# Optimization experiments

Measured on AMD Instinct MI355X. Metric: run time of the kernel, lower is better.

## Reference

```python
import jax, jax.numpy as jnp
import numpy as np

B, S0, S1 = 4, 768, 256
T = S0 + S1
D0, D1 = 2048, 1024
N, K, H = 8, 1, 256  # num_heads, num_kv_heads, head_dim
G = N // K
BIG_NEG = -2.3819763e38


def _apply_rope(x, positions, max_wavelength=10000):
    # x: [B, L, Hn, Hd]; positions: [B, L] float32
    half = x.shape[-1] // 2
    freq_exponents = (2.0 / x.shape[-1]) * jnp.arange(half, dtype=jnp.float32)
    timescale = max_wavelength ** freq_exponents
    radians = positions[..., None] / timescale[None, None, :]   # [B, L, half]
    radians = radians[..., None, :]                             # [B, L, 1, half]
    sin, cos = jnp.sin(radians), jnp.cos(radians)
    x1, x2 = jnp.split(x, 2, axis=-1)
    res = jnp.concatenate([x1 * cos - x2 * sin, x2 * cos + x1 * sin], axis=-1)
    return res.astype(x.dtype)


def setup_inputs() -> dict:
    key = jax.random.key(0)
    ks = jax.random.split(key, 8)
    x0 = jax.random.normal(ks[0], (B, S0, D0), dtype=jnp.float32)
    x1 = jax.random.normal(ks[1], (B, S1, D1), dtype=jnp.float32)
    positions = jnp.broadcast_to(jnp.arange(T, dtype=jnp.float32), (B, T))
    # causal mask [B, 1, T, T]
    attn_mask = jnp.broadcast_to(jnp.tril(jnp.ones((T, T), dtype=bool)), (B, 1, T, T))
    # lecun_normal-style init: std = 1/sqrt(fan_in=width)
    q0_w = jax.random.normal(ks[2], (N, D0, H), dtype=jnp.float32) * (D0 ** -0.5)
    kv0_w = jax.random.normal(ks[3], (2, K, D0, H), dtype=jnp.float32) * (D0 ** -0.5)
    q1_w = jax.random.normal(ks[4], (N, D1, H), dtype=jnp.float32) * (D1 ** -0.5)
    kv1_w = jax.random.normal(ks[5], (2, K, D1, H), dtype=jnp.float32) * (D1 ** -0.5)
    o0_w = jax.random.normal(ks[6], (N, H, D0), dtype=jnp.float32) * ((N * H) ** -0.5)
    o1_w = jax.random.normal(ks[7], (N, H, D1), dtype=jnp.float32) * ((N * H) ** -0.5)
    return {"x0": x0, "x1": x1, "positions": positions, "attn_mask": attn_mask,
            "q0_w": q0_w, "kv0_w": kv0_w, "q1_w": q1_w, "kv1_w": kv1_w,
            "o0_w": o0_w, "o1_w": o1_w}


def reference(x0, x1, positions, attn_mask, q0_w, kv0_w, q1_w, kv1_w, o0_w, o1_w):
    dtype = x0.dtype
    # per-stream GQA projections (num_kv_heads != num_heads path)
    q_a = jnp.einsum('BTD,NDH->BTNH', x0, q0_w)
    kv_a = jnp.einsum('BSD,CKDH->CBSKH', x0, kv0_w)
    q_b = jnp.einsum('BTD,NDH->BTNH', x1, q1_w)
    kv_b = jnp.einsum('BSD,CKDH->CBSKH', x1, kv1_w)
    # concat streams along sequence
    q = jnp.concatenate([q_a, q_b], axis=1)                 # [B, T, N, H]
    k = jnp.concatenate([kv_a[0], kv_b[0]], axis=1)         # [B, T, K, H]
    v = jnp.concatenate([kv_a[1], kv_b[1]], axis=1)         # [B, T, K, H]
    # inline RoPE + query scaling
    q = _apply_rope(q, positions) * (H ** -0.5)
    k = _apply_rope(k, positions)
    # GQA grouping: N = K * G
    qg = q.reshape(q.shape[0], q.shape[1], K, G, H)          # [B, T, K, G, H]
    logits = jnp.einsum('BTKGH,BSKH->BKGTS', qg, k,
                        preferred_element_type=jnp.float32)  # fp32 scores
    masked = jnp.where(attn_mask[:, :, None, :, :], logits, BIG_NEG)
    probs = jax.nn.softmax(masked, axis=-1).astype(dtype)
    encoded = jnp.einsum('BKGTS,BSKH->BTKGH', probs, v)
    encoded = encoded.reshape(encoded.shape[0], encoded.shape[1], N, H)  # [B, T, N, H]
    out0 = jnp.einsum('BTNH,NHD->BTD', encoded[:, :S0], o0_w)
    out1 = jnp.einsum('BTNH,NHD->BTD', encoded[:, S0:], o1_w)
    return (out0, out1)
```

## Files before the change

### kernel.cpp

```cpp
#include <hip/hip_runtime.h>

typedef unsigned short u16;
typedef __attribute__((ext_vector_type(8))) short bf16x8;
typedef __attribute__((ext_vector_type(4))) float f32x4;

#define CB   4
#define CS0  768
#define CS1  256
#define CT   1024
#define CD0  2048
#define CD1  1024
#define CN   8
#define CH   256
#define IDENT (1 << 30)
#define BIGBASE 0x7fffffff

__device__ __forceinline__ float bf2f(u16 u) {
    union { unsigned int i; float f; } v;
    v.i = ((unsigned int)u) << 16;
    return v.f;
}
__device__ __forceinline__ u16 f2bf(float f) {
    union { float f; unsigned int i; } v;
    v.f = f;
    unsigned int r = 0x7fffu + ((v.i >> 16) & 1u);
    return (u16)((v.i + r) >> 16);
}

__device__ __forceinline__ void gl_lds16(const u16* g, u16* lds_base) {
    __builtin_amdgcn_global_load_lds(
        (const __attribute__((address_space(1))) void*)g,
        (__attribute__((address_space(3))) void*)lds_base,
        16, 0, 0);
}

struct PSeg { const float* in; u16* out; int R, C, base, lgx, lgy, mode; };
struct PSeg8 { PSeg t[8]; };

__global__ __launch_bounds__(256) void prep_multi(PSeg8 segs)
{
    __shared__ float tl[2][32][33];
    int bid = blockIdx.x;
    PSeg g = segs.t[0];
    #pragma unroll
    for (int i = 1; i < 8; i++)
        if (bid >= segs.t[i].base) g = segs.t[i];
    int r = bid - g.base;
    int tid = threadIdx.x;
    if (g.mode == 0) {
        int i = r * 512 + tid;
        float4 v0 = ((const float4*)g.in)[i];
        float4 v1 = ((const float4*)g.in)[i + 256];
        ushort4 o0, o1;
        o0.x = f2bf(v0.x); o0.y = f2bf(v0.y); o0.z = f2bf(v0.z); o0.w = f2bf(v0.w);
        o1.x = f2bf(v1.x); o1.y = f2bf(v1.y); o1.z = f2bf(v1.z); o1.w = f2bf(v1.w);
        ((ushort4*)g.out)[i] = o0;
        ((ushort4*)g.out)[i + 256] = o1;
    } else {
        int bx  = r & ((1 << g.lgx) - 1);
        int byh = (r >> g.lgx) & ((1 << (g.lgy - 1)) - 1);
        int bz  = r >> (g.lgx + g.lgy - 1);
        const float* in = g.in + (size_t)bz * g.R * g.C;
        u16* out = g.out + (size_t)bz * g.R * g.C;
        int c0 = bx * 32, r0 = byh * 64;
        int lty = tid >> 3, ltx = tid & 7;
        #pragma unroll
        for (int tt = 0; tt < 2; tt++) {
            float4 v = *(const float4*)&in[(size_t)(r0 + tt * 32 + lty) * g.C + c0 + ltx * 4];
            tl[tt][lty][ltx * 4 + 0] = v.x;
            tl[tt][lty][ltx * 4 + 1] = v.y;
            tl[tt][lty][ltx * 4 + 2] = v.z;
            tl[tt][lty][ltx * 4 + 3] = v.w;
        }
        __syncthreads();
        int uy = tid >> 3, ux = tid & 7;
        int tt2 = ux >> 2, a0 = (ux & 3) * 8;
        bf16x8 ov;
        #pragma unroll
        for (int k = 0; k < 8; k++)
            ((u16*)&ov)[k] = f2bf(tl[tt2][a0 + k][uy]);
        *(bf16x8*)&out[(size_t)(c0 + uy) * g.R + r0 + ux * 8] = ov;
    }
}

struct GSeg {
    const u16* A; const u16* BT; void* C;
    int K, Cstride, base, lgnx;
    int Sa, Ta, ta, Sc, Tc, tc, obf, pad;
};
struct GSeg4 { GSeg s[4]; };

__global__ __launch_bounds__(256, 3) void gemm128_multi(GSeg4 segs)
{
    __shared__ __align__(16) u16 lds[3 * 8192];

    int bid = blockIdx.x;
    GSeg g = segs.s[0];
    if (bid >= segs.s[1].base) g = segs.s[1];
    if (bid >= segs.s[2].base) g = segs.s[2];
    if (bid >= segs.s[3].base) g = segs.s[3];

    int tid  = threadIdx.x;
    int r    = bid - g.base;
    int n0   = (r & ((1 << g.lgnx) - 1)) * 128;
    int m0   = (r >> g.lgnx) * 128;
    int wave = tid >> 6, lane = tid & 63;

    int srow  = tid >> 2;
    int skoff = ((tid & 3) ^ ((srow >> 1) & 3)) * 8;
    int am1 = m0 + srow, am2 = m0 + 64 + srow;
    const u16* aptr1 = g.A + (size_t)((am1 / g.Sa) * g.Ta + g.ta + am1 % g.Sa) * g.K + skoff;
    const u16* aptr2 = g.A + (size_t)((am2 / g.Sa) * g.Ta + g.ta + am2 % g.Sa) * g.K + skoff;
    const u16* bptr1 = g.BT + (size_t)(n0 + srow) * g.K + skoff;
    const u16* bptr2 = g.BT + (size_t)(n0 + 64 + srow) * g.K + skoff;

    int mw = (wave >> 1) * 64, nw = (wave & 1) * 64;
    int l15 = lane & 15;
    int q4  = lane >> 4;
    int sw  = (q4 ^ ((l15 >> 1) & 3)) * 8;

#define STAGE(bufi, tt) do { int kk = (tt) * 32; \
        u16* base = lds + (bufi) * 8192 + wave * 512; \
        gl_lds16(aptr1 + kk, base); \
        gl_lds16(aptr2 + kk, base + 2048); \
        gl_lds16(bptr1 + kk, base + 4096); \
        gl_lds16(bptr2 + kk, base + 6144); } while (0)

    f32x4 acc[4][4] = {};
    int nkt = g.K >> 5;

    STAGE(0, 0);
    STAGE(1, 1);

    int cur = 0, nxt = 2;
    for (int t = 0; t < nkt; ++t) {
        if (t + 1 < nkt) asm volatile("s_waitcnt vmcnt(4)" ::: "memory");
        else             asm volatile("s_waitcnt vmcnt(0)" ::: "memory");
        __builtin_amdgcn_sched_barrier(0);
        __builtin_amdgcn_s_barrier();
        asm volatile("" ::: "memory");
        if (t + 2 < nkt) STAGE(nxt, t + 2);

        const u16* At = lds + cur * 8192;
        const u16* Bt = At + 4096;
        bf16x8 af[4], bfr[4];
        #pragma unroll
        for (int i = 0; i < 4; i++)
            af[i] = *(const bf16x8*)&At[(mw + i * 16 + l15) * 32 + sw];
        #pragma unroll
        for (int i = 0; i < 4; i++)
            bfr[i] = *(const bf16x8*)&Bt[(nw + i * 16 + l15) * 32 + sw];
        asm volatile("s_waitcnt lgkmcnt(0)" ::: "memory");
        __builtin_amdgcn_sched_barrier(0);
        __builtin_amdgcn_s_setprio(1);
        #pragma unroll
        for (int mi = 0; mi < 4; mi++)
            #pragma unroll
            for (int ni = 0; ni < 4; ni++)
                acc[mi][ni] = __builtin_amdgcn_mfma_f32_16x16x32_bf16(
                    af[mi], bfr[ni], acc[mi][ni], 0, 0, 0);
        __builtin_amdgcn_s_setprio(0);
        cur = (cur == 2) ? 0 : cur + 1;
        nxt = (nxt == 2) ? 0 : nxt + 1;
    }
#undef STAGE

    #pragma unroll
    for (int mi = 0; mi < 4; mi++) {
        #pragma unroll
        for (int rr = 0; rr < 4; rr++) {
            int mm = m0 + mw + mi * 16 + q4 * 4 + rr;
            int grow = (mm / g.Sc) * g.Tc + g.tc + mm % g.Sc;
            if (g.obf) {
                u16* crow = (u16*)g.C + (size_t)grow * g.Cstride + n0 + nw + l15;
                #pragma unroll
                for (int ni = 0; ni < 4; ni++)
                    crow[ni * 16] = f2bf(acc[mi][ni][rr]);
            } else {
                float* crow = (float*)g.C + (size_t)grow * g.Cstride + n0 + nw + l15;
                #pragma unroll
                for (int ni = 0; ni < 4; ni++)
                    crow[ni * 16] = acc[mi][ni][rr];
            }
        }
    }
}

#define ROPE_L2 0.103810253f

__global__ __launch_bounds__(256) void rope_vt_kernel(
    const u16* __restrict__ kvsrc, const float* __restrict__ positions,
    u16* __restrict__ kb, u16* __restrict__ vto)
{
    int bid = blockIdx.x;
    if (bid < 2048) {
        int j  = bid * 256 + threadIdx.x;
        int h  = j & 127;
        int bt = j >> 7;
        const u16* base = kvsrc + (size_t)bt * 512;
        float pos = positions[bt];
        float rr  = pos * exp2f((float)h * -ROPE_L2);
        float sn = __sinf(rr), cs = __cosf(rr);
        float x1 = bf2f(base[h]), x2 = bf2f(base[h + 128]);
        int b = bt >> 10, t = bt & 1023;
        int h2 = h + 128;
        kb[((size_t)(b * 8 + (h  >> 5)) * 1024 + t) * 32 + (h  & 31)] = f2bf(x1 * cs - x2 * sn);
        kb[((size_t)(b * 8 + (h2 >> 5)) * 1024 + t) * 32 + (h2 & 31)] = f2bf(x2 * cs + x1 * sn);
    } else {
        int vb = bid - 2048;
        int h  = threadIdx.x;
        int sc = vb & 31;
        int b  = vb >> 5;
        const u16* src = kvsrc + ((size_t)(b * 1024 + sc * 32) * 512 + 256 + h);
        u16* dst = vto + ((size_t)(b * 32 + sc) * 256 + h) * 32;
        u16 buf[32];
        #pragma unroll
        for (int ss = 0; ss < 32; ss++)
            buf[ss] = src[(size_t)ss * 512];
        #pragma unroll
        for (int i = 0; i < 8; i++)
            ((ushort4*)dst)[i] = ((ushort4*)buf)[i];
    }
}

__global__ __launch_bounds__(256) void flash_attn(
    const u16* __restrict__ qraw, const u16* __restrict__ kb,
    const u16* __restrict__ vt, const float* __restrict__ positions,
    u16* __restrict__ encoded)
{
    __shared__ __align__(16) u16 Ks[8 * 64 * 32];
    __shared__ __align__(16) u16 Vs[2 * 256 * 32];
    __shared__ __align__(16) u16 Pw[4][16 * 72];

    int tid  = threadIdx.x;
    int wave = tid >> 6, lane = tid & 63;
    int q4 = lane >> 4, l15 = lane & 15;
    int swz = (q4 ^ ((l15 >> 1) & 3)) * 8;

    int bid  = blockIdx.x;
    int half = bid >> 8;
    int r    = bid & 255;
    int b    = (half << 1) | (r >> 7);
    int ti   = r & 127;
    if (half) ti = 127 - ti;
    int t0 = ti * 8;

    bf16x8 af[8];
    {
        int m = wave * 16 + l15;
        int head = m >> 3, tl = m & 7;
        const u16* qrow = qraw + ((size_t)(b * CT + t0 + tl) * 2048 + head * 256 + q4 * 8);
        #pragma unroll
        for (int kc = 0; kc < 8; kc++)
            af[kc] = *(const bf16x8*)(qrow + kc * 32);
        float pos = positions[b * CT + t0 + tl];
        #pragma unroll
        for (int kc = 0; kc < 4; kc++) {
            #pragma unroll
            for (int j = 0; j < 8; j++) {
                int h = kc * 32 + q4 * 8 + j;
                float ang = pos * exp2f((float)h * -ROPE_L2);
                float sn = __sinf(ang), cs = __cosf(ang);
                float x1 = bf2f(((u16*)&af[kc])[j]);
                float x2 = bf2f(((u16*)&af[kc + 4])[j]);
                ((u16*)&af[kc])[j]     = f2bf((x1 * cs - x2 * sn) * 0.0625f);
                ((u16*)&af[kc + 4])[j] = f2bf((x2 * cs + x1 * sn) * 0.0625f);
            }
        }
    }

    f32x4 O[16] = {};
    float lrun[4] = {0.f, 0.f, 0.f, 0.f};

    int send = t0 + 8;
    for (int s0 = 0; s0 < send; s0 += 64) {
        bool lastTile = (s0 + 64 >= send);
        if (s0) __syncthreads();
        #pragma unroll
        for (int is = 0; is < 8; is++) {
            int ubase = is * 256 + wave * 64;
            int u = ubase + lane;
            int s = (u >> 2) & 63, hc = u >> 8;
            int ug = (u & 3) ^ ((s >> 1) & 3);
            const u16* g = kb + ((size_t)((b * 8 + hc) * 1024 + s0 + s) * 32 + ug * 8);
            gl_lds16(g, Ks + (size_t)ubase * 8);
        }
        #pragma unroll
        for (int is = 0; is < 8; is++) {
            int ubase = is * 256 + wave * 64;
            int u = ubase + lane;
            int h = (u >> 2) & 255;
            int vg = (u & 3) ^ ((h >> 1) & 3);
            const u16* g = vt + ((size_t)(b * 32 + (s0 >> 5)) * 8192 + (size_t)(u >> 2) * 32 + vg * 8);
            gl_lds16(g, Vs + (size_t)ubase * 8);
        }
        __syncthreads();

        f32x4 P[4];
        #pragma unroll
        for (int ni = 0; ni < 4; ni++) {
            f32x4 c = {};
            #pragma unroll
            for (int kc = 0; kc < 8; kc++) {
                bf16x8 bfr = *(const bf16x8*)&Ks[kc * 2048 + (ni * 16 + l15) * 32 + swz];
                c = __builtin_amdgcn_mfma_f32_16x16x32_bf16(af[kc], bfr, c, 0, 0, 0);
            }
            P[ni] = c;
        }

        if (lastTile) {
            #pragma unroll
            for (int ni = 0; ni < 4; ni++)
                #pragma unroll
                for (int rr = 0; rr < 4; rr++) {
                    int trow = t0 + ((q4 * 4 + rr) & 7);
                    int scol = s0 + ni * 16 + l15;
                    if (scol > trow) P[ni][rr] = -3.0e38f;
                }
        }

        #pragma unroll
        for (int ni = 0; ni < 4; ni++)
            #pragma unroll
            for (int rr = 0; rr < 4; rr++) {
                float e = __expf(P[ni][rr]);
                P[ni][rr] = e;
                Pw[wave][(q4 * 4 + rr) * 72 + ni * 16 + l15] = f2bf(e);
            }
        #pragma unroll
        for (int rr = 0; rr < 4; rr++) {
            float s = (P[0][rr] + P[1][rr]) + (P[2][rr] + P[3][rr]);
            s += __shfl_xor(s, 1);
            s += __shfl_xor(s, 2);
            s += __shfl_xor(s, 4);
            s += __shfl_xor(s, 8);
            lrun[rr] += s;
        }

        bf16x8 pa0 = *(const bf16x8*)&Pw[wave][l15 * 72 + q4 * 8];
        bf16x8 pa1 = *(const bf16x8*)&Pw[wave][l15 * 72 + 32 + q4 * 8];
        #pragma unroll
        for (int nc = 0; nc < 16; nc++) {
            bf16x8 b0 = *(const bf16x8*)&Vs[(nc * 16 + l15) * 32 + swz];
            bf16x8 b1 = *(const bf16x8*)&Vs[8192 + (nc * 16 + l15) * 32 + swz];
            O[nc] = __builtin_amdgcn_mfma_f32_16x16x32_bf16(pa0, b0, O[nc], 0, 0, 0);
            O[nc] = __builtin_amdgcn_mfma_f32_16x16x32_bf16(pa1, b1, O[nc], 0, 0, 0);
        }
    }

    #pragma unroll
    for (int rr = 0; rr < 4; rr++) {
        int mm = wave * 16 + q4 * 4 + rr;
        int hd = mm >> 3, tl = mm & 7;
        u16* erow = encoded + ((size_t)(b * CT + t0 + tl) * 2048 + hd * 256 + l15);
        float inv = 1.0f / lrun[rr];
        #pragma unroll
        for (int nc = 0; nc < 16; nc++)
            erow[nc * 16] = f2bf(O[nc][rr] * inv);
    }
}

extern "C" void kernel_launch(void* const* d_in, const int* in_sizes, int n_in,
                              void* d_out, int out_size, void* d_ws, size_t ws_size,
                              hipStream_t stream)
{
    const float* x0        = (const float*)d_in[0];
    const float* x1        = (const float*)d_in[1];
    const float* positions = (const float*)d_in[2];
    const float* q0_w  = (const float*)d_in[4];
    const float* kv0_w = (const float*)d_in[5];
    const float* q1_w  = (const float*)d_in[6];
    const float* kv1_w = (const float*)d_in[7];
    const float* o0_w  = (const float*)d_in[8];
    const float* o1_w  = (const float*)d_in[9];
    float* out = (float*)d_out;

    char* W = (char*)d_ws;
    u16* qbuf16  = (u16*)(W);
    u16* kvbuf16 = (u16*)(W + 16777216);
    u16* WTo0  = (u16*)(W + 20971520);
    u16* WTo1  = (u16*)(W + 29360128);
    u16* x0b   = (u16*)(W + 33554432);
    u16* x1b   = (u16*)(W + 46137344);
    u16* WTq0  = (u16*)(W + 48234496);
    u16* WTkv0 = (u16*)(W + 56623104);
    u16* WTq1  = (u16*)(W + 58720256);
    u16* WTkv1 = (u16*)(W + 62914560);
    u16* kb  = WTkv0;
    u16* vtb = WTq1;
    u16* encoded = qbuf16;

    PSeg8 ps8;
    ps8.t[0] = { x0,    x0b,      0,    0,     0, 0, 0, 0 };
    ps8.t[1] = { x1,    x1b,      0,    0,  3072, 0, 0, 0 };
    ps8.t[2] = { q0_w,  WTq0,  2048,  256,  3584, 3, 6, 1 };
    ps8.t[3] = { kv0_w, WTkv0, 2048,  256,  5632, 3, 6, 1 };
    ps8.t[4] = { q1_w,  WTq1,  1024,  256,  6144, 3, 5, 1 };
    ps8.t[5] = { kv1_w, WTkv1, 1024,  256,  7168, 3, 5, 1 };
    ps8.t[6] = { o0_w,  WTo0,  2048, 2048,  7424, 6, 6, 1 };
    ps8.t[7] = { o1_w,  WTo1,  2048, 1024,  9472, 5, 6, 1 };
    prep_multi<<<dim3(10496), dim3(256), 0, stream>>>(ps8);

    GSeg4 ps;
    ps.s[0] = { x0b, WTq0,  qbuf16,  2048, 2048,   0, 4, IDENT, 0, 0, CS0, CT, 0,   1, 0 };
    ps.s[1] = { x0b, WTkv0, kvbuf16, 2048,  512, 384, 2, IDENT, 0, 0, CS0, CT, 0,   1, 0 };
    ps.s[2] = { x1b, WTq1,  qbuf16,  1024, 2048, 480, 4, IDENT, 0, 0, CS1, CT, CS0, 1, 0 };
    ps.s[3] = { x1b, WTkv1, kvbuf16, 1024,  512, 608, 2, IDENT, 0, 0, CS1, CT, CS0, 1, 0 };
    gemm128_multi<<<dim3(640), dim3(256), 0, stream>>>(ps);

    rope_vt_kernel<<<dim3(2176), dim3(256), 0, stream>>>(
        kvbuf16, positions, kb, vtb);

    flash_attn<<<dim3(512), dim3(256), 0, stream>>>(
        qbuf16, kb, vtb, positions, encoded);

    GSeg4 os;
    os.s[0] = { encoded, WTo0, out, 2048, 2048,   0, 4, CS0, CT, 0,   IDENT, 0, 0, 0, 0 };
    os.s[1] = { encoded, WTo1, out + (size_t)CB * CS0 * CD0,
                2048, 1024, 384, 3, CS1, CT, CS0, IDENT, 0, 0, 0, 0 };
    os.s[2] = { nullptr, nullptr, nullptr, 128, 0, BIGBASE, 0, 1, 0, 0, 1, 0, 0, 0, 0 };
    os.s[3] = { nullptr, nullptr, nullptr, 128, 0, BIGBASE, 0, 1, 0, 0, 1, 0, 0, 0, 0 };
    gemm128_multi<<<dim3(448), dim3(256), 0, stream>>>(os);
}
```

Baseline: 281.7 us.

## Fuse K RoPE and V transpose into KV projection GEMM epilogue

Removes the separate rope_vt_kernel by applying RoPE to K and writing the V-transposed layout directly from the KV projection GEMM epilogue. The K weight columns are interleaved during prep so each RoPE pair sits in adjacent lanes and can be exchanged with a shuffle. This cuts one kernel launch and a round trip of the KV buffer through memory. In exchange the epilogue does more per-element work (sin/cos per element) and uses scattered stores for K and V.

```diff
diff --git a/kernel.cpp b/kernel.cpp
--- a/kernel.cpp
+++ b/kernel.cpp
@@ -14,6 +14,7 @@
 #define CH   256
 #define IDENT (1 << 30)
 #define BIGBASE 0x7fffffff
+#define ROPE_L2 0.103810253f
 
 __device__ __forceinline__ float bf2f(u16 u) {
     union { unsigned int i; float f; } v;
@@ -79,14 +80,17 @@
         #pragma unroll
         for (int k = 0; k < 8; k++)
             ((u16*)&ov)[k] = f2bf(tl[tt2][a0 + k][uy]);
-        *(bf16x8*)&out[(size_t)(c0 + uy) * g.R + r0 + ux * 8] = ov;
+        int row = c0 + uy;
+        if (g.mode == 2 && bz == 0)
+            row = (row < 128) ? (row * 2) : ((row - 128) * 2 + 1);
+        *(bf16x8*)&out[(size_t)row * g.R + r0 + ux * 8] = ov;
     }
 }
 
 struct GSeg {
-    const u16* A; const u16* BT; void* C;
+    const u16* A; const u16* BT; void* C; const float* P; u16* V;
     int K, Cstride, base, lgnx;
-    int Sa, Ta, ta, Sc, Tc, tc, obf, pad;
+    int Sa, Ta, ta, Sc, Tc, tc, obf;
 };
 struct GSeg4 { GSeg s[4]; };
 
@@ -165,61 +169,69 @@
     }
 #undef STAGE
 
-    #pragma unroll
-    for (int mi = 0; mi < 4; mi++) {
-        #pragma unroll
-        for (int rr = 0; rr < 4; rr++) {
-            int mm = m0 + mw + mi * 16 + q4 * 4 + rr;
-            int grow = (mm / g.Sc) * g.Tc + g.tc + mm % g.Sc;
-            if (g.obf) {
-                u16* crow = (u16*)g.C + (size_t)grow * g.Cstride + n0 + nw + l15;
+    if (g.obf == 2) {
+        if (n0 < 256) {
+            #pragma unroll
+            for (int mi = 0; mi < 4; mi++) {
                 #pragma unroll
-                for (int ni = 0; ni < 4; ni++)
-                    crow[ni * 16] = f2bf(acc[mi][ni][rr]);
-            } else {
-                float* crow = (float*)g.C + (size_t)grow * g.Cstride + n0 + nw + l15;
+                for (int rr = 0; rr < 4; rr++) {
+                    int mm = m0 + mw + mi * 16 + q4 * 4 + rr;
+                    int grow = (mm / g.Sc) * g.Tc + g.tc + mm % g.Sc;
+                    int b = grow >> 10, t = grow & 1023;
+                    float pos = g.P[grow];
+                    #pragma unroll
+                    for (int ni = 0; ni < 4; ni++) {
+                        int c = n0 + nw + ni * 16 + l15;
+                        int m = c >> 1;
+                        float ang = pos * exp2f((float)m * -ROPE_L2);
+                        float sn = __sinf(ang), cs = __cosf(ang);
+                        float v = acc[mi][ni][rr];
+                        float p = __shfl_xor(v, 1);
+                        float o; int h;
+                        if (c & 1) { o = v * cs + p * sn; h = m + 128; }
+                        else       { o = v * cs - p * sn; h = m; }
+                        ((u16*)g.C)[((size_t)((b * 8 + (h >> 5)) * 1024 + t)) * 32 + (h & 31)] = f2bf(o);
+                    }
+                }
+            }
+        } else {
+            #pragma unroll
+            for (int mi = 0; mi < 4; mi++) {
+                int mm0 = m0 + mw + mi * 16 + q4 * 4;
+                int grow0 = (mm0 / g.Sc) * g.Tc + g.tc + mm0 % g.Sc;
+                int b = grow0 >> 10, t0 = grow0 & 1023;
                 #pragma unroll
-                for (int ni = 0; ni < 4; ni++)
-                    crow[ni * 16] = acc[mi][ni][rr];
-            }
-        }
-    }
-}
-
-#define ROPE_L2 0.103810253f
-
-__global__ __launch_bounds__(256) void rope_vt_kernel(
-    const u16* __restrict__ kvsrc, const float* __restrict__ positions,
-    u16* __restrict__ kb, u16* __restrict__ vto)
-{
-    int bid = blockIdx.x;
-    if (bid < 2048) {
-        int j  = bid * 256 + threadIdx.x;
-        int h  = j & 127;
-        int bt = j >> 7;
-        const u16* base = kvsrc + (size_t)bt * 512;
-        float pos = positions[bt];
-        float rr  = pos * exp2f((float)h * -ROPE_L2);
-        float sn = __sinf(rr), cs = __cosf(rr);
-        float x1 = bf2f(base[h]), x2 = bf2f(base[h + 128]);
-        int b = bt >> 10, t = bt & 1023;
-        int h2 = h + 128;
-        kb[((size_t)(b * 8 + (h  >> 5)) * 1024 + t) * 32 + (h  & 31)] = f2bf(x1 * cs - x2 * sn);
-        kb[((size_t)(b * 8 + (h2 >> 5)) * 1024 + t) * 32 + (h2 & 31)] = f2bf(x2 * cs + x1 * sn);
+                for (int ni = 0; ni < 4; ni++) {
+                    int h = n0 - 256 + nw + ni * 16 + l15;
+                    ushort4 o;
+                    o.x = f2bf(acc[mi][ni][0]);
+                    o.y = f2bf(acc[mi][ni][1]);
+                    o.z = f2bf(acc[mi][ni][2]);
+                    o.w = f2bf(acc[mi][ni][3]);
+                    *(ushort4*)&g.V[((size_t)((b * 32 + (t0 >> 5)) * 256 + h)) * 32 + (t0 & 31)] = o;
+                }
+            }
+        }
     } else {
-        int vb = bid - 2048;
-        int h  = threadIdx.x;
-        int sc = vb & 31;
-        int b  = vb >> 5;
-        const u16* src = kvsrc + ((size_t)(b * 1024 + sc * 32) * 512 + 256 + h);
-        u16* dst = vto + ((size_t)(b * 32 + sc) * 256 + h) * 32;
-        u16 buf[32];
-        #pragma unroll
-        for (int ss = 0; ss < 32; ss++)
-            buf[ss] = src[(size_t)ss * 512];
-        #pragma unroll
-        for (int i = 0; i < 8; i++)
-            ((ushort4*)dst)[i] = ((ushort4*)buf)[i];
+        #pragma unroll
+        for (int mi = 0; mi < 4; mi++) {
+            #pragma unroll
+            for (int rr = 0; rr < 4; rr++) {
+                int mm = m0 + mw + mi * 16 + q4 * 4 + rr;
+                int grow = (mm / g.Sc) * g.Tc + g.tc + mm % g.Sc;
+                if (g.obf) {
+                    u16* crow = (u16*)g.C + (size_t)grow * g.Cstride + n0 + nw + l15;
+                    #pragma unroll
+                    for (int ni = 0; ni < 4; ni++)
+                        crow[ni * 16] = f2bf(acc[mi][ni][rr]);
+                } else {
+                    float* crow = (float*)g.C + (size_t)grow * g.Cstride + n0 + nw + l15;
+                    #pragma unroll
+                    for (int ni = 0; ni < 4; ni++)
+                        crow[ni * 16] = acc[mi][ni][rr];
+                }
+            }
+        }
     }
 }
 
@@ -377,48 +389,44 @@
 
     char* W = (char*)d_ws;
     u16* qbuf16  = (u16*)(W);
-    u16* kvbuf16 = (u16*)(W + 16777216);
+    u16* kb      = (u16*)(W + 16777216);
+    u16* vtb     = (u16*)(W + 16777216 + 2097152);
     u16* WTo0  = (u16*)(W + 20971520);
     u16* WTo1  = (u16*)(W + 29360128);
     u16* x0b   = (u16*)(W + 33554432);
     u16* x1b   = (u16*)(W + 46137344);
     u16* WTq0  = (u16*)(W + 48234496);
     u16* WTkv0 = (u16*)(W + 56623104);
-    u16* WTq1  = (u16*)(W + 58720256);
-    u16* WTkv1 = (u16*)(W + 62914560);
-    u16* kb  = WTkv0;
-    u16* vtb = WTq1;
+    u16* WTkv1 = (u16*)(W + 58720256);
+    u16* WTq1  = (u16*)(W + 59768832);
     u16* encoded = qbuf16;
 
     PSeg8 ps8;
     ps8.t[0] = { x0,    x0b,      0,    0,     0, 0, 0, 0 };
     ps8.t[1] = { x1,    x1b,      0,    0,  3072, 0, 0, 0 };
     ps8.t[2] = { q0_w,  WTq0,  2048,  256,  3584, 3, 6, 1 };
-    ps8.t[3] = { kv0_w, WTkv0, 2048,  256,  5632, 3, 6, 1 };
+    ps8.t[3] = { kv0_w, WTkv0, 2048,  256,  5632, 3, 6, 2 };
     ps8.t[4] = { q1_w,  WTq1,  1024,  256,  6144, 3, 5, 1 };
-    ps8.t[5] = { kv1_w, WTkv1, 1024,  256,  7168, 3, 5, 1 };
+    ps8.t[5] = { kv1_w, WTkv1, 1024,  256,  7168, 3, 5, 2 };
     ps8.t[6] = { o0_w,  WTo0,  2048, 2048,  7424, 6, 6, 1 };
     ps8.t[7] = { o1_w,  WTo1,  2048, 1024,  9472, 5, 6, 1 };
     prep_multi<<<dim3(10496), dim3(256), 0, stream>>>(ps8);
 
     GSeg4 ps;
-    ps.s[0] = { x0b, WTq0,  qbuf16,  2048, 2048,   0, 4, IDENT, 0, 0, CS0, CT, 0,   1, 0 };
-    ps.s[1] = { x0b, WTkv0, kvbuf16, 2048,  512, 384, 2, IDENT, 0, 0, CS0, CT, 0,   1, 0 };
-    ps.s[2] = { x1b, WTq1,  qbuf16,  1024, 2048, 480, 4, IDENT, 0, 0, CS1, CT, CS0, 1, 0 };
-    ps.s[3] = { x1b, WTkv1, kvbuf16, 1024,  512, 608, 2, IDENT, 0, 0, CS1, CT, CS0, 1, 0 };
+    ps.s[0] = { x0b, WTq0,  qbuf16, nullptr,   nullptr, 2048, 2048,   0, 4, IDENT, 0, 0, CS0, CT, 0,   1 };
+    ps.s[1] = { x0b, WTkv0, kb,     positions, vtb,     2048,  512, 384, 2, IDENT, 0, 0, CS0, CT, 0,   2 };
+    ps.s[2] = { x1b, WTq1,  qbuf16, nullptr,   nullptr, 1024, 2048, 480, 4, IDENT, 0, 0, CS1, CT, CS0, 1 };
+    ps.s[3] = { x1b, WTkv1, kb,     positions, vtb,     1024,  512, 608, 2, IDENT, 0, 0, CS1, CT, CS0, 2 };
     gemm128_multi<<<dim3(640), dim3(256), 0, stream>>>(ps);
-
-    rope_vt_kernel<<<dim3(2176), dim3(256), 0, stream>>>(
-        kvbuf16, positions, kb, vtb);
 
     flash_attn<<<dim3(512), dim3(256), 0, stream>>>(
         qbuf16, kb, vtb, positions, encoded);
 
     GSeg4 os;
-    os.s[0] = { encoded, WTo0, out, 2048, 2048,   0, 4, CS0, CT, 0,   IDENT, 0, 0, 0, 0 };
-    os.s[1] = { encoded, WTo1, out + (size_t)CB * CS0 * CD0,
-                2048, 1024, 384, 3, CS1, CT, CS0, IDENT, 0, 0, 0, 0 };
-    os.s[2] = { nullptr, nullptr, nullptr, 128, 0, BIGBASE, 0, 1, 0, 0, 1, 0, 0, 0, 0 };
-    os.s[3] = { nullptr, nullptr, nullptr, 128, 0, BIGBASE, 0, 1, 0, 0, 1, 0, 0, 0, 0 };
+    os.s[0] = { encoded, WTo0, out, nullptr, nullptr, 2048, 2048,   0, 4, CS0, CT, 0,   IDENT, 0, 0, 0 };
+    os.s[1] = { encoded, WTo1, out + (size_t)CB * CS0 * CD0, nullptr, nullptr,
+                2048, 1024, 384, 3, CS1, CT, CS0, IDENT, 0, 0, 0 };
+    os.s[2] = { nullptr, nullptr, nullptr, nullptr, nullptr, 32, 0, BIGBASE, 0, 1, 0, 0, 1, 0, 0, 0 };
+    os.s[3] = { nullptr, nullptr, nullptr, nullptr, nullptr, 32, 0, BIGBASE, 0, 1, 0, 0, 1, 0, 0, 0 };
     gemm128_multi<<<dim3(448), dim3(256), 0, stream>>>(os);
 }
```

Result: no change. 278.5 us, median of 2 (-1.1%).
